# Performance work log

Hardware: AMD Instinct MI355X
Metric: run time of the kernel (lower is better)

Reference implementation:

```python
import jax, jax.numpy as jnp
import numpy as np

B, L, E, V, H, M, O = 16, 64, 256, 16000, 8, 4, 2
DH = E // H
START = 0

def _pe():
    pos = np.arange(L, dtype=np.float32)[:, None]
    div = np.exp(np.arange(0, E, 2, dtype=np.float32) * (-np.log(10000.0) / E))
    pe = np.zeros((L, E), dtype=np.float32)
    pe[:, 0::2] = np.sin(pos * div)
    pe[:, 1::2] = np.cos(pos * div)
    return jnp.asarray(pe)

PE = _pe()  # [L, E] sinusoidal positional encoding (dropout p=0.0)


def setup_inputs() -> dict:
    key = jax.random.key(0)
    ks = jax.random.split(key, 16)
    g = lambda k, sh, sc: jax.random.normal(k, sh, jnp.float32) * sc
    return {
        'noise': jax.random.normal(ks[0], (B, L), jnp.float32),
        'inEmb_W': g(ks[1], (M, L, L), 1.0 / np.sqrt(L)),   # M stacked Linear(L, L), [in,out] layout
        'inEmb_b': jnp.zeros((M, L), jnp.float32),
        'Wq': g(ks[2], (O, E, E), 1.0 / np.sqrt(E)),
        'bq': jnp.zeros((O, E), jnp.float32),
        'Wk': g(ks[3], (O, E, E), 1.0 / np.sqrt(E)),
        'bk': jnp.zeros((O, E), jnp.float32),
        'Wv': g(ks[4], (O, E, E), 1.0 / np.sqrt(E)),
        'bv': jnp.zeros((O, E), jnp.float32),
        'Wo': g(ks[5], (O, E, E), 1.0 / np.sqrt(E)),
        'bo': jnp.zeros((O, E), jnp.float32),
        'ln_g': jnp.ones((O, E), jnp.float32),
        'ln_b': jnp.zeros((O, E), jnp.float32),
        'emb': g(ks[6], (V, E), 1.0),                       # Word2Vec embedding table
        'soft_W': g(ks[7], (E, V), 1.0 / np.sqrt(E)),       # soft head Linear(E, V)
        'soft_b': jnp.zeros((V,), jnp.float32),
    }


def _ln(x, g, b):
    mu = x.mean(-1, keepdims=True)
    var = ((x - mu) ** 2).mean(-1, keepdims=True)
    return (x - mu) / jnp.sqrt(var + 1e-5) * g + b


def _mha_norm(kv, q, Wq, bq, Wk, bk, Wv, bv, Wo, bo, g, b, kmask):
    # MHAwithNorm: attn(query=q, key=kv, value=kv) -> out proj -> residual -> LayerNorm
    Q = (q @ Wq + bq).reshape(B, L, H, DH)
    K = (kv @ Wk + bk).reshape(B, L, H, DH)
    Vh = (kv @ Wv + bv).reshape(B, L, H, DH)
    s = jnp.einsum('bqhd,bkhd->bhqk', Q, K) / np.sqrt(DH)
    s = jnp.where(kmask[None, None, None, :], s, -1e9)  # only the tok generated positions are valid keys
    a = jax.nn.softmax(s, axis=-1)
    o = jnp.einsum('bhqk,bkhd->bqhd', a, Vh).reshape(B, L, E)
    return _ln(o @ Wo + bo + q, g, b)


def _decode(noise, inEmb_W, inEmb_b, Wq, bq, Wk, bk, Wv, bv, Wo, bo, ln_g, ln_b, emb, soft_W, soft_b):
    w = noise
    for i in range(M):
        w = w @ inEmb_W[i] + inEmb_b[i]
    w = jnp.broadcast_to(w[:, :, None], (B, L, E))  # unsqueeze(-1).repeat(1,1,E)

    Y0 = jnp.zeros((B, L, E), jnp.float32).at[:, 0].set(emb[START] + PE[0])

    def step(Y, tok):
        kmask = jnp.arange(L) < tok  # current sequence length == tok
        out = Y
        for i in range(O):  # cross-attn blocks against w[:, :tok]
            out = _mha_norm(w, out, Wq[i], bq[i], Wk[i], bk[i], Wv[i], bv[i], Wo[i], bo[i], ln_g[i], ln_b[i], kmask)
        for i in range(O):  # same blocks reused as self-attn (faithful to source)
            out = _mha_norm(out, out, Wq[i], bq[i], Wk[i], bk[i], Wv[i], bv[i], Wo[i], bo[i], ln_g[i], ln_b[i], kmask)
        logits = out[:, tok - 1] @ soft_W + soft_b
        probs = jax.nn.softmax(logits, axis=-1)
        nxt = jnp.argmax(probs, axis=-1)  # [B]
        Y = Y.at[:, tok].set(emb[nxt] + PE[tok])
        return Y, (nxt, probs)

    _, (toks, probs) = jax.lax.scan(step, Y0, jnp.arange(1, L))
    return toks, probs  # toks [L-1, B] int, probs [L-1, B, V]


def reference(noise, inEmb_W, inEmb_b, Wq, bq, Wk, bk, Wv, bv, Wo, bo, ln_g, ln_b, emb, soft_W, soft_b):
    toks, _ = _decode(noise, inEmb_W, inEmb_b, Wq, bq, Wk, bk, Wv, bv, Wo, bo, ln_g, ln_b, emb, soft_W, soft_b)
    # torch.stack(out_sent[0]): generated token ids of batch element 0, incl. <START>
    return jnp.concatenate([jnp.array([START], dtype=toks.dtype), toks[:, 0]])
```

## Files before the change

### kernel.cpp

```cpp
#include <hip/hip_runtime.h>
#include <stdint.h>


#define NWG 128
#define NT 256

__device__ __forceinline__ float ld_c(const float* p){
  return __hip_atomic_load(p, __ATOMIC_RELAXED, __HIP_MEMORY_SCOPE_AGENT);
}
__device__ __forceinline__ void st_c(float* p, float v){
  __hip_atomic_store(p, v, __ATOMIC_RELAXED, __HIP_MEMORY_SCOPE_AGENT);
}

__device__ __forceinline__ float wredsum(float v){
#pragma unroll
  for (int m=32;m;m>>=1) v += __shfl_xor(v,m,64);
  return v;
}
__device__ __forceinline__ float wredmax(float v){
#pragma unroll
  for (int m=32;m;m>>=1) v = fmaxf(v,__shfl_xor(v,m,64));
  return v;
}
__device__ __forceinline__ float g32sum(float v){
#pragma unroll
  for (int m=16;m;m>>=1) v += __shfl_xor(v,m,64);
  return v;
}
__device__ __forceinline__ float g32max(float v){
#pragma unroll
  for (int m=16;m;m>>=1) v = fmaxf(v,__shfl_xor(v,m,64));
  return v;
}
__device__ __forceinline__ unsigned long long shflx64(unsigned long long v,int m){
  unsigned int lo=(unsigned int)(v&0xffffffffull), hi=(unsigned int)(v>>32);
  lo=__shfl_xor(lo,m,64); hi=__shfl_xor(hi,m,64);
  return (((unsigned long long)hi)<<32)|(unsigned long long)lo;
}

__device__ __forceinline__ float pe_val(int l, int e){
  int j = e >> 1;
  float dv = expf((float)(2*j) * (-0.035977892078031970f));
  float arg = (float)l * dv;
  return (e & 1) ? cosf(arg) : sinf(arg);
}

__device__ __forceinline__ void gbar_f(int* arr, int* rel, int ep){
  __syncthreads();
  if (threadIdx.x==0){
    __builtin_amdgcn_fence(__ATOMIC_RELEASE, "agent");
    __hip_atomic_store(arr + blockIdx.x*16, ep, __ATOMIC_RELAXED, __HIP_MEMORY_SCOPE_AGENT);
  }
  if (blockIdx.x==0){
    if (threadIdx.x < NWG){
      while (__hip_atomic_load(arr + threadIdx.x*16, __ATOMIC_RELAXED, __HIP_MEMORY_SCOPE_AGENT) != ep)
        __builtin_amdgcn_s_sleep(1);
    }
    __syncthreads();
    if (threadIdx.x==0)
      __hip_atomic_store(rel, ep, __ATOMIC_RELAXED, __HIP_MEMORY_SCOPE_AGENT);
  }
  if (threadIdx.x==0){
    while (__hip_atomic_load(rel, __ATOMIC_RELAXED, __HIP_MEMORY_SCOPE_AGENT) != ep)
      __builtin_amdgcn_s_sleep(1);
    __builtin_amdgcn_fence(__ATOMIC_ACQUIRE, "agent");
  }
  __syncthreads();
}

__device__ __forceinline__ void gbar_nf(int* arr, int* rel, int ep){
  __syncthreads();
  if (threadIdx.x==0)
    __hip_atomic_store(arr + blockIdx.x*16, ep, __ATOMIC_RELAXED, __HIP_MEMORY_SCOPE_AGENT);
  if (blockIdx.x==0){
    if (threadIdx.x < NWG){
      while (__hip_atomic_load(arr + threadIdx.x*16, __ATOMIC_RELAXED, __HIP_MEMORY_SCOPE_AGENT) != ep)
        __builtin_amdgcn_s_sleep(1);
    }
    __syncthreads();
    if (threadIdx.x==0)
      __hip_atomic_store(rel, ep, __ATOMIC_RELAXED, __HIP_MEMORY_SCOPE_AGENT);
  }
  if (threadIdx.x==0){
    while (__hip_atomic_load(rel, __ATOMIC_RELAXED, __HIP_MEMORY_SCOPE_AGENT) != ep)
      __builtin_amdgcn_s_sleep(1);
  }
  __syncthreads();
}

extern "C" __global__ __launch_bounds__(256, 2)
void gen18124_kernel(const float* __restrict__ noise,
                     const float* __restrict__ iw, const float* __restrict__ ib,
                     const float* __restrict__ Wq, const float* __restrict__ bq,
                     const float* __restrict__ Wk, const float* __restrict__ bk,
                     const float* __restrict__ Wv, const float* __restrict__ bv,
                     const float* __restrict__ Wo, const float* __restrict__ bo,
                     const float* __restrict__ lng, const float* __restrict__ lnb,
                     const float* __restrict__ emb, const float* __restrict__ sw,
                     const float* __restrict__ sb,
                     int* __restrict__ out, float* __restrict__ ws)
{
  const float ISQ = 0.17677669529663687f;
  __shared__ float sm[5376];
  __shared__ unsigned long long redU[4];
  extern __shared__ float swl[];

  float* WVEC = ws;
  float* SKC  = ws+64;
  float* SVC  = ws+576;
  float* KAP  = ws+1088;
  float* UT   = ws+5184;
  float* CC   = ws+9280;
  float* BETA = ws+9792;
  unsigned long long* SLOT = (unsigned long long*)(ws+9808);
  int* ARR = (int*)(ws+9824);
  int* REL = (int*)(ws+11872);
  float* Yg  = ws+11876;
  float* R1  = ws+28260;
  float* QB  = ws+44644;
  float* KB  = ws+61028;
  float* VB  = ws+77412;
  float* R2  = ws+93796;
  float* Z2P = ws+110180;
  float* Z3P = ws+241252;

  const int g = blockIdx.x, t = threadIdx.x;
  int ep = 0;

  {
    const int base = g*125;
#pragma unroll 8
    for (int i=t; i<256*128; i+=NT){
      int e=i>>7, c=i&127;
      float val = 0.f;
      if (c<125) val = sw[e*16000 + base + c];
      swl[i]=val;
    }
  }

  {
    int c0 = 2*g;
    float a0=Wk[t*256+c0],       a1=Wk[t*256+c0+1];
    float a2=Wk[65536+t*256+c0], a3=Wk[65536+t*256+c0+1];
    float a4=Wv[t*256+c0],       a5=Wv[t*256+c0+1];
    float a6=Wv[65536+t*256+c0], a7=Wv[65536+t*256+c0+1];
    a0=wredsum(a0); a1=wredsum(a1); a2=wredsum(a2); a3=wredsum(a3);
    a4=wredsum(a4); a5=wredsum(a5); a6=wredsum(a6); a7=wredsum(a7);
    int lane=t&63, wid=t>>6;
    if (lane==0){
      sm[wid*8+0]=a0; sm[wid*8+1]=a1; sm[wid*8+2]=a2; sm[wid*8+3]=a3;
      sm[wid*8+4]=a4; sm[wid*8+5]=a5; sm[wid*8+6]=a6; sm[wid*8+7]=a7;
    }
    __syncthreads();
    if (t<8){
      float s=sm[t]+sm[8+t]+sm[16+t]+sm[24+t];
      if (t<4) SKC[(t>>1)*256 + c0 + (t&1)] = s;
      else     SVC[((t-4)>>1)*256 + c0 + ((t-4)&1)] = s;
    }
    __syncthreads();
    if (g==0){
      float* wl = sm+64;
      if (t<64) wl[t] = noise[t];
      __syncthreads();
      for (int i=0;i<4;i++){
        float acc=0.f;
        if (t<64){
          for (int in_=0;in_<64;in_++) acc += wl[in_]*iw[(i*64+in_)*64+t];
          acc += ib[i*64+t];
        }
        __syncthreads();
        if (t<64) wl[t]=acc;
        __syncthreads();
      }
      if (t<64) WVEC[t]=wl[t];
      if (t==0) *SLOT = 0ull;
    }
    if (g==1){
      Yg[t] = emb[t] + pe_val(0,t);
      if (t==0) out[0]=0;
    }
  }
  gbar_f(ARR,REL,++ep);

  {
    int c0 = 2*g;
    float p00 = bv[t]    *Wo[t*256+c0],        p01 = bv[t]    *Wo[t*256+c0+1];
    float p10 = bv[256+t]*Wo[65536+t*256+c0],  p11 = bv[256+t]*Wo[65536+t*256+c0+1];
    p00=wredsum(p00); p01=wredsum(p01); p10=wredsum(p10); p11=wredsum(p11);
    int lane=t&63, wid=t>>6;
    if (lane==0){ sm[wid*4+0]=p00; sm[wid*4+1]=p01; sm[wid*4+2]=p10; sm[wid*4+3]=p11; }
    __syncthreads();
    if (t<4){
      float s=sm[t]+sm[4+t]+sm[8+t]+sm[12+t];
      int i=t>>1, cl=t&1;
      CC[i*256+c0+cl] = s + bo[i*256+c0+cl];
    }
    if (t<32){
      int i=t>>4, h=(t>>1)&7, c=c0+(t&1);
      float s=0.f;
      for (int e2=0;e2<32;e2++) s += SVC[i*256+h*32+e2]*Wo[i*65536+(h*32+e2)*256+c];
      UT[(i*8+h)*256+c]=s;
    }
    if (t>=32 && t<64){
      int u=t-32, i=u>>4, h=(u>>1)&7, e=c0+(u&1);
      float s=0.f;
      for (int c2=0;c2<32;c2++) s += Wq[i*65536+e*256+h*32+c2]*SKC[i*256+h*32+c2];
      KAP[(i*8+h)*256+e]=s;
    }
    if (g==0 && t>=64 && t<80){
      int u=t-64, i=u>>3, h=u&7;
      float s=0.f;
      for (int c2=0;c2<32;c2++) s += bq[i*256+h*32+c2]*SKC[i*256+h*32+c2];
      BETA[i*8+h]=s;
    }
  }
  gbar_f(ARR,REL,++ep);

  for (int tok=1; tok<64; tok++){
    const int n = tok-1;

    if (g < tok){
      const int q = g;
      float* xrow = sm; float* rrow = sm+256; float* m8 = sm+512; float* redv = sm+528;
      if (q==n && tok>1){
        unsigned long long s = __hip_atomic_load(SLOT, __ATOMIC_RELAXED, __HIP_MEMORY_SCOPE_AGENT);
        int v = (int)(~(unsigned int)(s & 0xffffffffull));
        if (t==0) out[q]=v;
        float yv = emb[v*256+t] + pe_val(q,t);
        xrow[t]=yv; st_c(&Yg[q*256+t], yv);
      } else {
        xrow[t]=ld_c(&Yg[q*256+t]);
      }
      __syncthreads();
      for (int blk=0; blk<2; blk++){
        const float* src = blk ? rrow : xrow;
        int h=t>>5, j=t&31;
        float part=0.f;
        for (int jj=j; jj<256; jj+=32) part += src[jj]*KAP[(blk*8+h)*256+jj];
        part = g32sum(part);
        float alpha = (part + BETA[blk*8+h]) * ISQ;
        float s1 = (j<tok)     ? alpha*WVEC[j]    : -3.4e38f;
        float s2 = (j+32<tok)  ? alpha*WVEC[j+32] : -3.4e38f;
        float mx = g32max(fmaxf(s1,s2));
        float e1 = expf(s1-mx), e2 = expf(s2-mx);
        float sn = e1*((j<tok)?WVEC[j]:0.f) + e2*((j+32<tok)?WVEC[j+32]:0.f);
        float sd = e1+e2;
        sn=g32sum(sn); sd=g32sum(sd);
        if (j==0) m8[h]=sn/sd;
        __syncthreads();
        float x_ = blk ? rrow[t] : xrow[t];
        float z = CC[blk*256+t] + x_;
#pragma unroll
        for (int h2=0;h2<8;h2++) z += m8[h2]*UT[(blk*8+h2)*256+t];
        float ssum=wredsum(z), ssq=wredsum(z*z);
        int lane=t&63, wid=t>>6;
        if (lane==0){ redv[wid]=ssum; redv[4+wid]=ssq; }
        __syncthreads();
        float ts=redv[0]+redv[1]+redv[2]+redv[3];
        float tq=redv[4]+redv[5]+redv[6]+redv[7];
        float mu=ts*(1.f/256.f);
        float var=tq*(1.f/256.f)-mu*mu;
        float rstd=1.f/sqrtf(var+1e-5f);
        float rv=(z-mu)*rstd*lng[blk*256+t]+lnb[blk*256+t];
        __syncthreads();
        rrow[t]=rv;
        __syncthreads();
      }
      st_c(&R1[q*256+t], rrow[t]);
    }
    gbar_nf(ARR,REL,++ep);

    {
      if (g==0 && t==0) __hip_atomic_store(SLOT, 0ull, __ATOMIC_RELAXED, __HIP_MEMORY_SCOPE_AGENT);
      const int h=g&7, rg=g>>3;
      float* rows4 = sm;
#pragma unroll
      for (int jj=0;jj<4;jj++) rows4[jj*256+t] = ld_c(&R1[(rg+16*jj)*256+t]);
      __syncthreads();
      int c=t&31, epp=t>>5;
      const int col=h*32+c;
      float aq[4]={0,0,0,0}, ak[4]={0,0,0,0}, av[4]={0,0,0,0};
#pragma unroll 8
      for (int e=epp*32; e<epp*32+32; e++){
        float wq_=Wq[e*256+col], wk_=Wk[e*256+col], wv_=Wv[e*256+col];
#pragma unroll
        for (int jj=0;jj<4;jj++){ float r=rows4[jj*256+e]; aq[jj]+=r*wq_; ak[jj]+=r*wk_; av[jj]+=r*wv_; }
      }
#pragma unroll
      for (int jj=0;jj<4;jj++){
        aq[jj]+=__shfl_xor(aq[jj],32,64);
        ak[jj]+=__shfl_xor(ak[jj],32,64);
        av[jj]+=__shfl_xor(av[jj],32,64);
      }
      float4* redq=(float4*)(sm+1056); float4* redk=(float4*)(sm+1568); float4* redv4=(float4*)(sm+2080);
      int lane=t&63, wid=t>>6;
      if (lane<32){
        redq[wid*32+lane]=make_float4(aq[0],aq[1],aq[2],aq[3]);
        redk[wid*32+lane]=make_float4(ak[0],ak[1],ak[2],ak[3]);
        redv4[wid*32+lane]=make_float4(av[0],av[1],av[2],av[3]);
      }
      __syncthreads();
      if (t<32){
        float4 A=redq[t],B4=redq[32+t],C4=redq[64+t],D4=redq[96+t];
        float sq[4]={A.x+B4.x+C4.x+D4.x, A.y+B4.y+C4.y+D4.y, A.z+B4.z+C4.z+D4.z, A.w+B4.w+C4.w+D4.w};
        A=redk[t];B4=redk[32+t];C4=redk[64+t];D4=redk[96+t];
        float sk[4]={A.x+B4.x+C4.x+D4.x, A.y+B4.y+C4.y+D4.y, A.z+B4.z+C4.z+D4.z, A.w+B4.w+C4.w+D4.w};
        A=redv4[t];B4=redv4[32+t];C4=redv4[64+t];D4=redv4[96+t];
        float sv[4]={A.x+B4.x+C4.x+D4.x, A.y+B4.y+C4.y+D4.y, A.z+B4.z+C4.z+D4.z, A.w+B4.w+C4.w+D4.w};
        int cc=h*32+t;
        float bq_=bq[cc], bk_=bk[cc], bv_=bv[cc];
#pragma unroll
        for (int jj=0;jj<4;jj++){
          int q_=rg+16*jj;
          if (q_<tok){
            st_c(&QB[q_*256+cc], sq[jj]+bq_);
            st_c(&KB[q_*256+cc], sk[jj]+bk_);
            st_c(&VB[q_*256+cc], sv[jj]+bv_);
          }
        }
      }
    }
    gbar_nf(ARR,REL,++ep);

    {
      const int h=g&7, rg=g>>3;
      float* Ks=sm; float* Vs=sm+2112; float* qrow=sm+4224; float* arow=sm+4352; float* o2s=sm+4608;
      int k=t>>2, f0=(t&3)*8;
      if (k<tok){
#pragma unroll
        for (int i2=0;i2<8;i2++){
          Ks[k*33+f0+i2]=ld_c(&KB[k*256+h*32+f0+i2]);
          Vs[k*33+f0+i2]=ld_c(&VB[k*256+h*32+f0+i2]);
        }
      }
      if (t<128){ int jj=t>>5, c=t&31; int q_=rg+16*jj; if (q_<tok) qrow[jj*32+c]=ld_c(&QB[q_*256+h*32+c]); }
      __syncthreads();
      int w=t>>6, lane=t&63; int q_=rg+16*w; bool ok=q_<tok;
      float sc=-3.4e38f;
      if (ok && lane<tok){
        sc=0.f;
#pragma unroll
        for (int c2=0;c2<32;c2++) sc+=qrow[w*32+c2]*Ks[lane*33+c2];
        sc*=ISQ;
      }
      float mx=wredmax(sc);
      float ex=(ok&&lane<tok)? expf(sc-mx):0.f;
      float sd=wredsum(ex);
      arow[w*64+lane]= ok ? ex/sd : 0.f;
      __syncthreads();
      int j=lane&31, half=lane>>5;
      float oa=0.f;
      if (ok){ for (int k2=half;k2<tok;k2+=2) oa+=arow[w*64+k2]*Vs[k2*33+j]; }
      oa += __shfl_xor(oa,32,64);
      if (lane<32) o2s[w*32+j]=oa;
      __syncthreads();
      float acc[4]={0,0,0,0};
#pragma unroll 8
      for (int j2=0;j2<32;j2++){
        float wv_=Wo[(h*32+j2)*256+t];
#pragma unroll
        for (int jj=0;jj<4;jj++) acc[jj]+=o2s[jj*32+j2]*wv_;
      }
#pragma unroll
      for (int jj=0;jj<4;jj++){ int q2=rg+16*jj; if (q2<tok) st_c(&Z2P[(h*64+q2)*256+t], acc[jj]); }
    }
    gbar_nf(ARR,REL,++ep);

    {
      const int h=g&7, rg=g>>3;
      float* rows4=sm; float* mus=sm+1024;
#pragma unroll
      for (int jj=0;jj<4;jj++){
        int q_=rg+16*jj;
        float z = bo[t] + ld_c(&R1[q_*256+t]);
#pragma unroll
        for (int h2=0;h2<8;h2++) z += ld_c(&Z2P[(h2*64+q_)*256+t]);
        rows4[jj*256+t]=z;
      }
      __syncthreads();
      {
        int w=t>>6, lane=t&63;
        float v0=rows4[w*256+lane], v1=rows4[w*256+64+lane], v2=rows4[w*256+128+lane], v3=rows4[w*256+192+lane];
        float s=v0+v1+v2+v3, sq2=v0*v0+v1*v1+v2*v2+v3*v3;
        s=wredsum(s); sq2=wredsum(sq2);
        if (lane==0){
          float mu=s*(1.f/256.f);
          float var=sq2*(1.f/256.f)-mu*mu;
          mus[w*2]=mu; mus[w*2+1]=1.f/sqrtf(var+1e-5f);
        }
      }
      __syncthreads();
#pragma unroll
      for (int jj=0;jj<4;jj++){
        float mu=mus[jj*2], rstd=mus[jj*2+1];
        float val=(rows4[jj*256+t]-mu)*rstd*lng[t]+lnb[t];
        rows4[jj*256+t]=val;
        int q_=rg+16*jj;
        if (h==0 && q_<tok) st_c(&R2[q_*256+t], val);
      }
      __syncthreads();
      int c=t&31, epp=t>>5;
      const int col=h*32+c;
      float aq[4]={0,0,0,0}, ak[4]={0,0,0,0}, av[4]={0,0,0,0};
#pragma unroll 8
      for (int e=epp*32; e<epp*32+32; e++){
        float wq_=Wq[65536+e*256+col], wk_=Wk[65536+e*256+col], wv_=Wv[65536+e*256+col];
#pragma unroll
        for (int jj=0;jj<4;jj++){ float r=rows4[jj*256+e]; aq[jj]+=r*wq_; ak[jj]+=r*wk_; av[jj]+=r*wv_; }
      }
#pragma unroll
      for (int jj=0;jj<4;jj++){
        aq[jj]+=__shfl_xor(aq[jj],32,64);
        ak[jj]+=__shfl_xor(ak[jj],32,64);
        av[jj]+=__shfl_xor(av[jj],32,64);
      }
      float4* redq=(float4*)(sm+1056); float4* redk=(float4*)(sm+1568); float4* redv4=(float4*)(sm+2080);
      int lane=t&63, wid=t>>6;
      if (lane<32){
        redq[wid*32+lane]=make_float4(aq[0],aq[1],aq[2],aq[3]);
        redk[wid*32+lane]=make_float4(ak[0],ak[1],ak[2],ak[3]);
        redv4[wid*32+lane]=make_float4(av[0],av[1],av[2],av[3]);
      }
      __syncthreads();
      if (t<32){
        float4 A=redq[t],B4=redq[32+t],C4=redq[64+t],D4=redq[96+t];
        float sq[4]={A.x+B4.x+C4.x+D4.x, A.y+B4.y+C4.y+D4.y, A.z+B4.z+C4.z+D4.z, A.w+B4.w+C4.w+D4.w};
        A=redk[t];B4=redk[32+t];C4=redk[64+t];D4=redk[96+t];
        float sk[4]={A.x+B4.x+C4.x+D4.x, A.y+B4.y+C4.y+D4.y, A.z+B4.z+C4.z+D4.z, A.w+B4.w+C4.w+D4.w};
        A=redv4[t];B4=redv4[32+t];C4=redv4[64+t];D4=redv4[96+t];
        float sv[4]={A.x+B4.x+C4.x+D4.x, A.y+B4.y+C4.y+D4.y, A.z+B4.z+C4.z+D4.z, A.w+B4.w+C4.w+D4.w};
        int cc=h*32+t;
#pragma unroll
        for (int jj=0;jj<4;jj++){
          int q_=rg+16*jj;
          if (q_<tok){
            st_c(&KB[q_*256+cc], sk[jj]+bk[256+cc]);
            st_c(&VB[q_*256+cc], sv[jj]+bv[256+cc]);
            if (q_==n) st_c(&QB[q_*256+cc], sq[jj]+bq[256+cc]);
          }
        }
      }
    }
    gbar_nf(ARR,REL,++ep);

    {
      const int h=g&7, rg=g>>3;
      if (rg == (n&15)){
        float* Ks=sm; float* Vs=sm+2112; float* qn=sm+4224; float* arow=sm+4352; float* o3s=sm+4608;
        int k=t>>2, f0=(t&3)*8;
        if (k<tok){
#pragma unroll
          for (int i2=0;i2<8;i2++){
            Ks[k*33+f0+i2]=ld_c(&KB[k*256+h*32+f0+i2]);
            Vs[k*33+f0+i2]=ld_c(&VB[k*256+h*32+f0+i2]);
          }
        }
        if (t<32) qn[t]=ld_c(&QB[n*256+h*32+t]);
        __syncthreads();
        int lane=t&63, w=t>>6;
        if (w==0){
          float sc=-3.4e38f;
          if (lane<tok){
            sc=0.f;
#pragma unroll
            for (int c2=0;c2<32;c2++) sc+=qn[c2]*Ks[lane*33+c2];
            sc*=ISQ;
          }
          float mx=wredmax(sc);
          float ex=(lane<tok)? expf(sc-mx):0.f;
          float sd=wredsum(ex);
          arow[lane]=ex/sd;
        }
        __syncthreads();
        if (w==0){
          int j=lane&31, half=lane>>5;
          float oa=0.f;
          for (int k2=half;k2<tok;k2+=2) oa+=arow[k2]*Vs[k2*33+j];
          oa+=__shfl_xor(oa,32,64);
          if (lane<32) o3s[j]=oa;
        }
        __syncthreads();
        float acc=0.f;
#pragma unroll 8
        for (int j2=0;j2<32;j2++) acc+=o3s[j2]*Wo[65536+(h*32+j2)*256+t];
        st_c(&Z3P[h*256+t], acc);
      }
    }
    gbar_nf(ARR,REL,++ep);

    {
      float* outn=sm; float* redv=sm+256; float* pp=sm+512;
      float z = bo[256+t] + ld_c(&R2[n*256+t]);
#pragma unroll
      for (int h2=0;h2<8;h2++) z += ld_c(&Z3P[h2*256+t]);
      float s=wredsum(z), sq2=wredsum(z*z);
      int lane=t&63, wid=t>>6;
      if (lane==0){ redv[wid]=s; redv[4+wid]=sq2; }
      __syncthreads();
      float ts=redv[0]+redv[1]+redv[2]+redv[3];
      float tq=redv[4]+redv[5]+redv[6]+redv[7];
      float mu=ts*(1.f/256.f);
      float var=tq*(1.f/256.f)-mu*mu;
      float rstd=1.f/sqrtf(var+1e-5f);
      outn[t]=(z-mu)*rstd*lng[256+t]+lnb[256+t];
      __syncthreads();
      const int c = t & 127, half = t >> 7;
      float acc = 0.f;
      if (c < 125){
        const int e0 = half*128;
#pragma unroll 8
        for (int e=e0; e<e0+128; e++) acc += outn[e]*swl[e*128+c];
      }
      if (half==1 && c<125) pp[c]=acc;
      __syncthreads();
      unsigned long long key=0ull;
      if (half==0 && c<125){
        int v=g*125+c;
        float a2 = acc + pp[c] + sb[v];
        unsigned int fb=__float_as_uint(a2);
        fb = (fb&0x80000000u)? ~fb : (fb|0x80000000u);
        key=(((unsigned long long)fb)<<32) | (unsigned long long)(~(unsigned int)v);
      }
#pragma unroll
      for (int m=32;m;m>>=1){
        unsigned long long o=shflx64(key,m);
        key = (o>key)? o : key;
      }
      if (lane==0) redU[wid]=key;
      __syncthreads();
      if (t==0){
        unsigned long long kk=redU[0];
        if (redU[1]>kk) kk=redU[1];
        if (redU[2]>kk) kk=redU[2];
        if (redU[3]>kk) kk=redU[3];
        atomicMax(SLOT, kk);
      }
    }
    gbar_nf(ARR,REL,++ep);
  }

  if (g==0 && t==0){
    unsigned long long s=__hip_atomic_load(SLOT,__ATOMIC_RELAXED,__HIP_MEMORY_SCOPE_AGENT);
    out[63]=(int)(~(unsigned int)(s&0xffffffffull));
  }
}

extern "C" void kernel_launch(void* const* d_in, const int* in_sizes, int n_in,
                              void* d_out, int out_size, void* d_ws, size_t ws_size,
                              hipStream_t stream)
{
  (void)in_sizes; (void)n_in; (void)out_size; (void)ws_size;
  hipLaunchKernelGGL(gen18124_kernel, dim3(NWG), dim3(NT), 131072, stream,
    (const float*)d_in[0],  (const float*)d_in[1],  (const float*)d_in[2],
    (const float*)d_in[3],  (const float*)d_in[4],  (const float*)d_in[5],
    (const float*)d_in[6],  (const float*)d_in[7],  (const float*)d_in[8],
    (const float*)d_in[9],  (const float*)d_in[10], (const float*)d_in[11],
    (const float*)d_in[12], (const float*)d_in[13], (const float*)d_in[14],
    (const float*)d_in[15], (int*)d_out, (float*)d_ws);
}
```

Measured before the change: 4.291 ms.

## Replace grid-wide barriers with per-XCD local barriers and replicated work

Within each decode step, the grid-wide barriers are replaced by per-XCD barriers. Each XCD's workgroups redundantly compute the full QKV/attention/LN pipeline, striding over rows by their slot within the XCD, so synchronisation stays inside one chiplet's L2. Only the vocab argmax is combined across XCDs, through a global max slot and a counter that one workgroup per XCD waits on. This is meant to cut cross-chiplet barrier latency. The cost is duplicated compute per XCD and fewer workgroups sharing each phase, and it relies on workgroup-scope atomics being coherent within an XCD.

```diff
diff --git a/kernel.cpp b/kernel.cpp
--- a/kernel.cpp
+++ b/kernel.cpp
@@ -4,12 +4,32 @@
 
 #define NWG 128
 #define NT 256
-
-__device__ __forceinline__ float ld_c(const float* p){
-  return __hip_atomic_load(p, __ATOMIC_RELAXED, __HIP_MEMORY_SCOPE_AGENT);
-}
-__device__ __forceinline__ void st_c(float* p, float v){
-  __hip_atomic_store(p, v, __ATOMIC_RELAXED, __HIP_MEMORY_SCOPE_AGENT);
+#define AS __ATOMIC_RELAXED
+
+typedef unsigned long long u64;
+
+__device__ __forceinline__ float ld1(const float* p){
+  return __hip_atomic_load(p, AS, __HIP_MEMORY_SCOPE_AGENT);
+}
+__device__ __forceinline__ void st1(float* p, float v){
+  __hip_atomic_store(p, v, AS, __HIP_MEMORY_SCOPE_AGENT);
+}
+__device__ __forceinline__ int ldi1(const int* p){
+  return __hip_atomic_load(p, AS, __HIP_MEMORY_SCOPE_AGENT);
+}
+
+__device__ __forceinline__ void larrive(int* line){
+  __hip_atomic_fetch_add(line, 1, AS, __HIP_MEMORY_SCOPE_WORKGROUP);
+}
+__device__ __forceinline__ int lcasread(int* line, int tgt){
+  int e = tgt;
+  __hip_atomic_compare_exchange_strong(line, &e, tgt, AS, AS, __HIP_MEMORY_SCOPE_WORKGROUP);
+  return e;
+}
+__device__ __forceinline__ int get_xcc(){
+  int x;
+  asm volatile("s_getreg_b32 %0, hwreg(HW_REG_XCC_ID)" : "=s"(x));
+  return x & 7;
 }
 
 __device__ __forceinline__ float wredsum(float v){
@@ -32,12 +52,11 @@
   for (int m=16;m;m>>=1) v = fmaxf(v,__shfl_xor(v,m,64));
   return v;
 }
-__device__ __forceinline__ unsigned long long shflx64(unsigned long long v,int m){
+__device__ __forceinline__ u64 shflx64(u64 v,int m){
   unsigned int lo=(unsigned int)(v&0xffffffffull), hi=(unsigned int)(v>>32);
   lo=__shfl_xor(lo,m,64); hi=__shfl_xor(hi,m,64);
-  return (((unsigned long long)hi)<<32)|(unsigned long long)lo;
-}
-
+  return (((u64)hi)<<32)|(u64)lo;
+}
 __device__ __forceinline__ float pe_val(int l, int e){
   int j = e >> 1;
   float dv = expf((float)(2*j) * (-0.035977892078031970f));
@@ -49,41 +68,30 @@
   __syncthreads();
   if (threadIdx.x==0){
     __builtin_amdgcn_fence(__ATOMIC_RELEASE, "agent");
-    __hip_atomic_store(arr + blockIdx.x*16, ep, __ATOMIC_RELAXED, __HIP_MEMORY_SCOPE_AGENT);
+    __hip_atomic_store(arr + blockIdx.x*16, ep, AS, __HIP_MEMORY_SCOPE_AGENT);
   }
   if (blockIdx.x==0){
     if (threadIdx.x < NWG){
-      while (__hip_atomic_load(arr + threadIdx.x*16, __ATOMIC_RELAXED, __HIP_MEMORY_SCOPE_AGENT) != ep)
+      while (__hip_atomic_load(arr + threadIdx.x*16, AS, __HIP_MEMORY_SCOPE_AGENT) != ep)
         __builtin_amdgcn_s_sleep(1);
     }
     __syncthreads();
     if (threadIdx.x==0)
-      __hip_atomic_store(rel, ep, __ATOMIC_RELAXED, __HIP_MEMORY_SCOPE_AGENT);
+      __hip_atomic_store(rel, ep, AS, __HIP_MEMORY_SCOPE_AGENT);
   }
   if (threadIdx.x==0){
-    while (__hip_atomic_load(rel, __ATOMIC_RELAXED, __HIP_MEMORY_SCOPE_AGENT) != ep)
+    while (__hip_atomic_load(rel, AS, __HIP_MEMORY_SCOPE_AGENT) != ep)
       __builtin_amdgcn_s_sleep(1);
     __builtin_amdgcn_fence(__ATOMIC_ACQUIRE, "agent");
   }
   __syncthreads();
 }
 
-__device__ __forceinline__ void gbar_nf(int* arr, int* rel, int ep){
+__device__ __forceinline__ void lbar(int* line, int tgt){
   __syncthreads();
-  if (threadIdx.x==0)
-    __hip_atomic_store(arr + blockIdx.x*16, ep, __ATOMIC_RELAXED, __HIP_MEMORY_SCOPE_AGENT);
-  if (blockIdx.x==0){
-    if (threadIdx.x < NWG){
-      while (__hip_atomic_load(arr + threadIdx.x*16, __ATOMIC_RELAXED, __HIP_MEMORY_SCOPE_AGENT) != ep)
-        __builtin_amdgcn_s_sleep(1);
-    }
-    __syncthreads();
-    if (threadIdx.x==0)
-      __hip_atomic_store(rel, ep, __ATOMIC_RELAXED, __HIP_MEMORY_SCOPE_AGENT);
-  }
   if (threadIdx.x==0){
-    while (__hip_atomic_load(rel, __ATOMIC_RELAXED, __HIP_MEMORY_SCOPE_AGENT) != ep)
-      __builtin_amdgcn_s_sleep(1);
+    larrive(line);
+    while (lcasread(line, tgt) < tgt) __builtin_amdgcn_s_sleep(1);
   }
   __syncthreads();
 }
@@ -102,7 +110,8 @@
 {
   const float ISQ = 0.17677669529663687f;
   __shared__ float sm[5376];
-  __shared__ unsigned long long redU[4];
+  __shared__ u64 redU[4];
+  __shared__ int s_xcd, s_slot, s_win;
   extern __shared__ float swl[];
 
   float* WVEC = ws;
@@ -112,7 +121,6 @@
   float* UT   = ws+5184;
   float* CC   = ws+9280;
   float* BETA = ws+9792;
-  unsigned long long* SLOT = (unsigned long long*)(ws+9808);
   int* ARR = (int*)(ws+9824);
   int* REL = (int*)(ws+11872);
   float* Yg  = ws+11876;
@@ -123,6 +131,15 @@
   float* R2  = ws+93796;
   float* Z2P = ws+110180;
   float* Z3P = ws+241252;
+  float* KB2 = ws+243300;
+  float* VB2 = ws+259684;
+  float* Q2N = ws+276068;
+  int*  XCDC = (int*)(ws+280000);
+  int*  ARRL = (int*)(ws+280128);
+  int*  WINA = (int*)(ws+280256);
+  int*  DCNT = (int*)(ws+280384);
+  u64*  GMAX = (u64*)(ws+280400);
+  u64*  SLOT64 = (u64*)(ws+281424);
 
   const int g = blockIdx.x, t = threadIdx.x;
   int ep = 0;
@@ -139,6 +156,11 @@
   }
 
   {
+    if (g==2){
+      if (t<64) __hip_atomic_store(&SLOT64[t], 0ull, AS, __HIP_MEMORY_SCOPE_AGENT);
+      if (t==64) __hip_atomic_store(DCNT, 0, AS, __HIP_MEMORY_SCOPE_AGENT);
+      if (t>=128 && t<256) __hip_atomic_store(&XCDC[t-128], 0, AS, __HIP_MEMORY_SCOPE_AGENT);
+    }
     int c0 = 2*g;
     float a0=Wk[t*256+c0],       a1=Wk[t*256+c0+1];
     float a2=Wk[65536+t*256+c0], a3=Wk[65536+t*256+c0+1];
@@ -173,7 +195,6 @@
         __syncthreads();
       }
       if (t<64) WVEC[t]=wl[t];
-      if (t==0) *SLOT = 0ull;
     }
     if (g==1){
       Yg[t] = emb[t] + pe_val(0,t);
@@ -183,6 +204,17 @@
   gbar_f(ARR,REL,++ep);
 
   {
+    if (t==0){
+      int x = get_xcc();
+      s_xcd = x;
+      s_slot = __hip_atomic_fetch_add(&XCDC[x*16], 1, AS, __HIP_MEMORY_SCOPE_AGENT);
+    }
+    __syncthreads();
+    int xcd = s_xcd, slot = s_slot;
+    if (slot==0){
+      if (t<64) __hip_atomic_exchange(&GMAX[xcd*64+t], 0ull, AS, __HIP_MEMORY_SCOPE_WORKGROUP);
+      if (t==64) __hip_atomic_exchange(&ARRL[xcd*16], 0, AS, __HIP_MEMORY_SCOPE_WORKGROUP);
+    }
     int c0 = 2*g;
     float p00 = bv[t]    *Wo[t*256+c0],        p01 = bv[t]    *Wo[t*256+c0+1];
     float p10 = bv[256+t]*Wo[65536+t*256+c0],  p11 = bv[256+t]*Wo[65536+t*256+c0+1];
@@ -216,20 +248,34 @@
   }
   gbar_f(ARR,REL,++ep);
 
+  const int xcd = s_xcd, slot = s_slot;
+  int cnt = ldi1(&XCDC[xcd*16]);
+  int G = 0;
+#pragma unroll
+  for (int x=0;x<8;x++) G += (ldi1(&XCDC[x*16]) > 0) ? 1 : 0;
+  int* myARR = &ARRL[xcd*16];
+  int lphase = 0;
+
   for (int tok=1; tok<64; tok++){
     const int n = tok-1;
 
-    if (g < tok){
-      const int q = g;
+    for (int q = slot; q < tok; q += cnt){
+      __syncthreads();
       float* xrow = sm; float* rrow = sm+256; float* m8 = sm+512; float* redv = sm+528;
-      if (q==n && tok>1){
-        unsigned long long s = __hip_atomic_load(SLOT, __ATOMIC_RELAXED, __HIP_MEMORY_SCOPE_AGENT);
-        int v = (int)(~(unsigned int)(s & 0xffffffffull));
-        if (t==0) out[q]=v;
+      bool isnew = (q==n && tok>1);
+      if (isnew && t==0){
+        int e0 = 0;
+        __hip_atomic_compare_exchange_strong(&WINA[xcd*16], &e0, 0, AS, AS, __HIP_MEMORY_SCOPE_WORKGROUP);
+        s_win = e0;
+        out[q] = e0;
+      }
+      __syncthreads();
+      if (isnew){
+        int v = s_win;
         float yv = emb[v*256+t] + pe_val(q,t);
-        xrow[t]=yv; st_c(&Yg[q*256+t], yv);
+        xrow[t]=yv; st1(&Yg[q*256+t], yv);
       } else {
-        xrow[t]=ld_c(&Yg[q*256+t]);
+        xrow[t]=ld1(&Yg[q*256+t]);
       }
       __syncthreads();
       for (int blk=0; blk<2; blk++){
@@ -266,16 +312,17 @@
         rrow[t]=rv;
         __syncthreads();
       }
-      st_c(&R1[q*256+t], rrow[t]);
-    }
-    gbar_nf(ARR,REL,++ep);
-
-    {
-      if (g==0 && t==0) __hip_atomic_store(SLOT, 0ull, __ATOMIC_RELAXED, __HIP_MEMORY_SCOPE_AGENT);
-      const int h=g&7, rg=g>>3;
+      st1(&R1[q*256+t], rrow[t]);
+    }
+    lbar(myARR, cnt*(++lphase));
+
+    for (int vg = slot; vg < 128; vg += cnt){
+      const int h=vg&7, rg=vg>>3;
+      if (rg >= tok) continue;
+      __syncthreads();
       float* rows4 = sm;
 #pragma unroll
-      for (int jj=0;jj<4;jj++) rows4[jj*256+t] = ld_c(&R1[(rg+16*jj)*256+t]);
+      for (int jj=0;jj<4;jj++) rows4[jj*256+t] = ld1(&R1[(rg+16*jj)*256+t]);
       __syncthreads();
       int c=t&31, epp=t>>5;
       const int col=h*32+c;
@@ -313,91 +360,94 @@
         for (int jj=0;jj<4;jj++){
           int q_=rg+16*jj;
           if (q_<tok){
-            st_c(&QB[q_*256+cc], sq[jj]+bq_);
-            st_c(&KB[q_*256+cc], sk[jj]+bk_);
-            st_c(&VB[q_*256+cc], sv[jj]+bv_);
+            st1(&QB[q_*256+cc], sq[jj]+bq_);
+            st1(&KB[q_*256+cc], sk[jj]+bk_);
+            st1(&VB[q_*256+cc], sv[jj]+bv_);
           }
         }
       }
     }
-    gbar_nf(ARR,REL,++ep);
+    lbar(myARR, cnt*(++lphase));
 
     {
-      const int h=g&7, rg=g>>3;
       float* Ks=sm; float* Vs=sm+2112; float* qrow=sm+4224; float* arow=sm+4352; float* o2s=sm+4608;
-      int k=t>>2, f0=(t&3)*8;
-      if (k<tok){
-#pragma unroll
-        for (int i2=0;i2<8;i2++){
-          Ks[k*33+f0+i2]=ld_c(&KB[k*256+h*32+f0+i2]);
-          Vs[k*33+f0+i2]=ld_c(&VB[k*256+h*32+f0+i2]);
-        }
-      }
-      if (t<128){ int jj=t>>5, c=t&31; int q_=rg+16*jj; if (q_<tok) qrow[jj*32+c]=ld_c(&QB[q_*256+h*32+c]); }
-      __syncthreads();
-      int w=t>>6, lane=t&63; int q_=rg+16*w; bool ok=q_<tok;
-      float sc=-3.4e38f;
-      if (ok && lane<tok){
-        sc=0.f;
-#pragma unroll
-        for (int c2=0;c2<32;c2++) sc+=qrow[w*32+c2]*Ks[lane*33+c2];
-        sc*=ISQ;
-      }
-      float mx=wredmax(sc);
-      float ex=(ok&&lane<tok)? expf(sc-mx):0.f;
-      float sd=wredsum(ex);
-      arow[w*64+lane]= ok ? ex/sd : 0.f;
-      __syncthreads();
-      int j=lane&31, half=lane>>5;
-      float oa=0.f;
-      if (ok){ for (int k2=half;k2<tok;k2+=2) oa+=arow[w*64+k2]*Vs[k2*33+j]; }
-      oa += __shfl_xor(oa,32,64);
-      if (lane<32) o2s[w*32+j]=oa;
-      __syncthreads();
-      float acc[4]={0,0,0,0};
+      int lasth = -1;
+      for (int vg = slot; vg < 128; vg += cnt){
+        const int h=vg&7, rg=vg>>3;
+        if (rg >= tok) continue;
+        if (h != lasth){
+          __syncthreads();
+          int k=t>>2, f0=(t&3)*8;
+          if (k<tok){
+#pragma unroll
+            for (int i2=0;i2<8;i2++){
+              Ks[k*33+f0+i2]=ld1(&KB[k*256+h*32+f0+i2]);
+              Vs[k*33+f0+i2]=ld1(&VB[k*256+h*32+f0+i2]);
+            }
+          }
+          lasth=h;
+        }
+        __syncthreads();
+        if (t<128){ int jj=t>>5, c=t&31; int q_=rg+16*jj; if (q_<tok) qrow[jj*32+c]=ld1(&QB[q_*256+h*32+c]); }
+        __syncthreads();
+        int w=t>>6, lane=t&63; int q_=rg+16*w; bool ok=q_<tok;
+        float sc=-3.4e38f;
+        if (ok && lane<tok){
+          sc=0.f;
+#pragma unroll
+          for (int c2=0;c2<32;c2++) sc+=qrow[w*32+c2]*Ks[lane*33+c2];
+          sc*=ISQ;
+        }
+        float mx=wredmax(sc);
+        float ex=(ok&&lane<tok)? expf(sc-mx):0.f;
+        float sd=wredsum(ex);
+        arow[w*64+lane]= ok ? ex/sd : 0.f;
+        __syncthreads();
+        int j=lane&31, half=lane>>5;
+        float oa=0.f;
+        if (ok){ for (int k2=half;k2<tok;k2+=2) oa+=arow[w*64+k2]*Vs[k2*33+j]; }
+        oa += __shfl_xor(oa,32,64);
+        if (lane<32) o2s[w*32+j]=oa;
+        __syncthreads();
+        float acc[4]={0,0,0,0};
 #pragma unroll 8
-      for (int j2=0;j2<32;j2++){
-        float wv_=Wo[(h*32+j2)*256+t];
-#pragma unroll
-        for (int jj=0;jj<4;jj++) acc[jj]+=o2s[jj*32+j2]*wv_;
-      }
-#pragma unroll
-      for (int jj=0;jj<4;jj++){ int q2=rg+16*jj; if (q2<tok) st_c(&Z2P[(h*64+q2)*256+t], acc[jj]); }
-    }
-    gbar_nf(ARR,REL,++ep);
-
-    {
-      const int h=g&7, rg=g>>3;
-      float* rows4=sm; float* mus=sm+1024;
-#pragma unroll
-      for (int jj=0;jj<4;jj++){
-        int q_=rg+16*jj;
-        float z = bo[t] + ld_c(&R1[q_*256+t]);
-#pragma unroll
-        for (int h2=0;h2<8;h2++) z += ld_c(&Z2P[(h2*64+q_)*256+t]);
-        rows4[jj*256+t]=z;
-      }
-      __syncthreads();
-      {
-        int w=t>>6, lane=t&63;
-        float v0=rows4[w*256+lane], v1=rows4[w*256+64+lane], v2=rows4[w*256+128+lane], v3=rows4[w*256+192+lane];
-        float s=v0+v1+v2+v3, sq2=v0*v0+v1*v1+v2*v2+v3*v3;
-        s=wredsum(s); sq2=wredsum(sq2);
-        if (lane==0){
-          float mu=s*(1.f/256.f);
-          float var=sq2*(1.f/256.f)-mu*mu;
-          mus[w*2]=mu; mus[w*2+1]=1.f/sqrtf(var+1e-5f);
-        }
-      }
-      __syncthreads();
-#pragma unroll
-      for (int jj=0;jj<4;jj++){
-        float mu=mus[jj*2], rstd=mus[jj*2+1];
-        float val=(rows4[jj*256+t]-mu)*rstd*lng[t]+lnb[t];
-        rows4[jj*256+t]=val;
-        int q_=rg+16*jj;
-        if (h==0 && q_<tok) st_c(&R2[q_*256+t], val);
-      }
+        for (int j2=0;j2<32;j2++){
+          float wv_=Wo[(h*32+j2)*256+t];
+#pragma unroll
+          for (int jj=0;jj<4;jj++) acc[jj]+=o2s[jj*32+j2]*wv_;
+        }
+#pragma unroll
+        for (int jj=0;jj<4;jj++){ int q2=rg+16*jj; if (q2<tok) st1(&Z2P[(h*64+q2)*256+t], acc[jj]); }
+      }
+    }
+    lbar(myARR, cnt*(++lphase));
+
+    for (int q = slot; q < tok; q += cnt){
+      __syncthreads();
+      float* redv = sm+528;
+      float z = bo[t] + ld1(&R1[q*256+t]);
+#pragma unroll
+      for (int h2=0;h2<8;h2++) z += ld1(&Z2P[(h2*64+q)*256+t]);
+      float ssum=wredsum(z), ssq=wredsum(z*z);
+      int lane=t&63, wid=t>>6;
+      if (lane==0){ redv[wid]=ssum; redv[4+wid]=ssq; }
+      __syncthreads();
+      float ts=redv[0]+redv[1]+redv[2]+redv[3];
+      float tq=redv[4]+redv[5]+redv[6]+redv[7];
+      float mu=ts*(1.f/256.f);
+      float var=tq*(1.f/256.f)-mu*mu;
+      float rstd=1.f/sqrtf(var+1e-5f);
+      st1(&R2[q*256+t], (z-mu)*rstd*lng[t]+lnb[t]);
+    }
+    lbar(myARR, cnt*(++lphase));
+
+    for (int vg = slot; vg < 128; vg += cnt){
+      const int h=vg&7, rg=vg>>3;
+      if (rg >= tok) continue;
+      __syncthreads();
+      float* rows4 = sm;
+#pragma unroll
+      for (int jj=0;jj<4;jj++) rows4[jj*256+t] = ld1(&R2[(rg+16*jj)*256+t]);
       __syncthreads();
       int c=t&31, epp=t>>5;
       const int col=h*32+c;
@@ -434,65 +484,66 @@
         for (int jj=0;jj<4;jj++){
           int q_=rg+16*jj;
           if (q_<tok){
-            st_c(&KB[q_*256+cc], sk[jj]+bk[256+cc]);
-            st_c(&VB[q_*256+cc], sv[jj]+bv[256+cc]);
-            if (q_==n) st_c(&QB[q_*256+cc], sq[jj]+bq[256+cc]);
+            st1(&KB2[q_*256+cc], sk[jj]+bk[256+cc]);
+            st1(&VB2[q_*256+cc], sv[jj]+bv[256+cc]);
+            if (q_==n) st1(&Q2N[cc], sq[jj]+bq[256+cc]);
           }
         }
       }
     }
-    gbar_nf(ARR,REL,++ep);
+    lbar(myARR, cnt*(++lphase));
+
+    for (int vg = slot; vg < 128; vg += cnt){
+      if ((vg>>3) != (n&15)) continue;
+      const int h=vg&7;
+      __syncthreads();
+      float* Ks=sm; float* Vs=sm+2112; float* qn=sm+4224; float* arow=sm+4352; float* o3s=sm+4608;
+      int k=t>>2, f0=(t&3)*8;
+      if (k<tok){
+#pragma unroll
+        for (int i2=0;i2<8;i2++){
+          Ks[k*33+f0+i2]=ld1(&KB2[k*256+h*32+f0+i2]);
+          Vs[k*33+f0+i2]=ld1(&VB2[k*256+h*32+f0+i2]);
+        }
+      }
+      if (t<32) qn[t]=ld1(&Q2N[h*32+t]);
+      __syncthreads();
+      int lane=t&63, w=t>>6;
+      if (w==0){
+        float sc=-3.4e38f;
+        if (lane<tok){
+          sc=0.f;
+#pragma unroll
+          for (int c2=0;c2<32;c2++) sc+=qn[c2]*Ks[lane*33+c2];
+          sc*=ISQ;
+        }
+        float mx=wredmax(sc);
+        float ex=(lane<tok)? expf(sc-mx):0.f;
+        float sd=wredsum(ex);
+        arow[lane]=ex/sd;
+      }
+      __syncthreads();
+      if (w==0){
+        int j=lane&31, half=lane>>5;
+        float oa=0.f;
+        for (int k2=half;k2<tok;k2+=2) oa+=arow[k2]*Vs[k2*33+j];
+        oa+=__shfl_xor(oa,32,64);
+        if (lane<32) o3s[j]=oa;
+      }
+      __syncthreads();
+      float acc=0.f;
+#pragma unroll 8
+      for (int j2=0;j2<32;j2++) acc+=o3s[j2]*Wo[65536+(h*32+j2)*256+t];
+      st1(&Z3P[h*256+t], acc);
+    }
+    lbar(myARR, cnt*(++lphase));
 
     {
-      const int h=g&7, rg=g>>3;
-      if (rg == (n&15)){
-        float* Ks=sm; float* Vs=sm+2112; float* qn=sm+4224; float* arow=sm+4352; float* o3s=sm+4608;
-        int k=t>>2, f0=(t&3)*8;
-        if (k<tok){
-#pragma unroll
-          for (int i2=0;i2<8;i2++){
-            Ks[k*33+f0+i2]=ld_c(&KB[k*256+h*32+f0+i2]);
-            Vs[k*33+f0+i2]=ld_c(&VB[k*256+h*32+f0+i2]);
-          }
-        }
-        if (t<32) qn[t]=ld_c(&QB[n*256+h*32+t]);
-        __syncthreads();
-        int lane=t&63, w=t>>6;
-        if (w==0){
-          float sc=-3.4e38f;
-          if (lane<tok){
-            sc=0.f;
-#pragma unroll
-            for (int c2=0;c2<32;c2++) sc+=qn[c2]*Ks[lane*33+c2];
-            sc*=ISQ;
-          }
-          float mx=wredmax(sc);
-          float ex=(lane<tok)? expf(sc-mx):0.f;
-          float sd=wredsum(ex);
-          arow[lane]=ex/sd;
-        }
-        __syncthreads();
-        if (w==0){
-          int j=lane&31, half=lane>>5;
-          float oa=0.f;
-          for (int k2=half;k2<tok;k2+=2) oa+=arow[k2]*Vs[k2*33+j];
-          oa+=__shfl_xor(oa,32,64);
-          if (lane<32) o3s[j]=oa;
-        }
-        __syncthreads();
-        float acc=0.f;
-#pragma unroll 8
-        for (int j2=0;j2<32;j2++) acc+=o3s[j2]*Wo[65536+(h*32+j2)*256+t];
-        st_c(&Z3P[h*256+t], acc);
-      }
-    }
-    gbar_nf(ARR,REL,++ep);
-
-    {
+      __syncthreads();
       float* outn=sm; float* redv=sm+256; float* pp=sm+512;
-      float z = bo[256+t] + ld_c(&R2[n*256+t]);
-#pragma unroll
-      for (int h2=0;h2<8;h2++) z += ld_c(&Z3P[h2*256+t]);
+      float z = bo[256+t] + ld1(&R2[n*256+t]);
+#pragma unroll
+      for (int h2=0;h2<8;h2++) z += ld1(&Z3P[h2*256+t]);
       float s=wredsum(z), sq2=wredsum(z*z);
       int lane=t&63, wid=t>>6;
       if (lane==0){ redv[wid]=s; redv[4+wid]=sq2; }
@@ -513,35 +564,44 @@
       }
       if (half==1 && c<125) pp[c]=acc;
       __syncthreads();
-      unsigned long long key=0ull;
+      u64 key=0ull;
       if (half==0 && c<125){
         int v=g*125+c;
         float a2 = acc + pp[c] + sb[v];
         unsigned int fb=__float_as_uint(a2);
         fb = (fb&0x80000000u)? ~fb : (fb|0x80000000u);
-        key=(((unsigned long long)fb)<<32) | (unsigned long long)(~(unsigned int)v);
+        key=(((u64)fb)<<32) | (u64)(~(unsigned int)v);
       }
 #pragma unroll
       for (int m=32;m;m>>=1){
-        unsigned long long o=shflx64(key,m);
+        u64 o=shflx64(key,m);
         key = (o>key)? o : key;
       }
       if (lane==0) redU[wid]=key;
       __syncthreads();
       if (t==0){
-        unsigned long long kk=redU[0];
+        u64 kk=redU[0];
         if (redU[1]>kk) kk=redU[1];
         if (redU[2]>kk) kk=redU[2];
         if (redU[3]>kk) kk=redU[3];
-        atomicMax(SLOT, kk);
-      }
-    }
-    gbar_nf(ARR,REL,++ep);
-  }
-
-  if (g==0 && t==0){
-    unsigned long long s=__hip_atomic_load(SLOT,__ATOMIC_RELAXED,__HIP_MEMORY_SCOPE_AGENT);
-    out[63]=(int)(~(unsigned int)(s&0xffffffffull));
+        __hip_atomic_fetch_max(&GMAX[xcd*64+tok], kk, AS, __HIP_MEMORY_SCOPE_WORKGROUP);
+      }
+    }
+    lbar(myARR, cnt*(++lphase));
+
+    if (slot==0 && t==0){
+      u64 e0 = 0ull;
+      __hip_atomic_compare_exchange_strong(&GMAX[xcd*64+tok], &e0, 0ull, AS, AS, __HIP_MEMORY_SCOPE_WORKGROUP);
+      __hip_atomic_fetch_max(&SLOT64[tok], e0, AS, __HIP_MEMORY_SCOPE_AGENT);
+      __hip_atomic_fetch_add(DCNT, 1, AS, __HIP_MEMORY_SCOPE_AGENT);
+      while (__hip_atomic_load(DCNT, AS, __HIP_MEMORY_SCOPE_AGENT) < G*tok)
+        __builtin_amdgcn_s_sleep(1);
+      u64 sf = __hip_atomic_load(&SLOT64[tok], AS, __HIP_MEMORY_SCOPE_AGENT);
+      int v = (int)(~(unsigned int)(sf & 0xffffffffull));
+      __hip_atomic_exchange(&WINA[xcd*16], v, AS, __HIP_MEMORY_SCOPE_WORKGROUP);
+      if (tok==63) out[63]=v;
+    }
+    lbar(myARR, cnt*(++lphase));
   }
 }
 
```

Measured after the change: 9.825 ms. 129% more time.
